# Kernel optimization log

Measured on AMD Instinct MI355X. Metric: run time of the kernel, lower is better.

## Reference

```python
import jax, jax.numpy as jnp
import numpy as np

N_NODES = 50000
N_EDGES = 800000
IN_CH = 128
OUT_CH = 128
LN_EPS = 1e-5


def setup_inputs() -> dict:
    key = jax.random.key(0)
    k1, k2, k3, k4 = jax.random.split(key, 4)
    x = jax.random.normal(k1, (N_NODES, IN_CH), dtype=jnp.float32)
    edge_index = jax.random.randint(k2, (2, N_EDGES), 0, N_NODES, dtype=jnp.int64)
    # GCNConv linear weight (glorot-ish scale) and bias
    W = jax.random.normal(k3, (IN_CH, OUT_CH), dtype=jnp.float32) * (1.0 / np.sqrt(IN_CH))
    b = jnp.zeros((OUT_CH,), dtype=jnp.float32)
    # LayerNorm affine params
    ln_w = jnp.ones((OUT_CH,), dtype=jnp.float32)
    ln_b = jnp.zeros((OUT_CH,), dtype=jnp.float32)
    del k4
    return {"x": x, "edge_index": edge_index, "W": W, "b": b, "ln_w": ln_w, "ln_b": ln_b}


def reference(x, edge_index, W, b, ln_w, ln_b):
    N = x.shape[0]
    # --- GCNConv: add self loops, symmetric normalization, scatter-add ---
    loop = jnp.arange(N, dtype=edge_index.dtype)
    row = jnp.concatenate([edge_index[0], loop])  # source nodes (x_j)
    col = jnp.concatenate([edge_index[1], loop])  # target nodes (aggregate here)
    h = x @ W  # [N, out]
    deg = jax.ops.segment_sum(jnp.ones(row.shape[0], dtype=h.dtype), col, num_segments=N)
    dinv = jnp.where(deg > 0, jax.lax.rsqrt(deg), 0.0)
    norm = dinv[row] * dinv[col]  # [E+N]
    msg = h[row] * norm[:, None]  # gather + scale
    out = jax.ops.segment_sum(msg, col, num_segments=N) + b  # scatter-add + bias
    # --- LayerNorm over feature dim ---
    mu = jnp.mean(out, axis=-1, keepdims=True)
    var = jnp.mean(jnp.square(out - mu), axis=-1, keepdims=True)
    out = (out - mu) * jax.lax.rsqrt(var + LN_EPS) * ln_w + ln_b
    # --- ReLU; dropout is identity in eval mode ---
    return jax.nn.relu(out)
```

## Files before the change

kernel.cpp:

```cpp
#include <hip/hip_runtime.h>
#include <hip/hip_bf16.h>

#define CH 128
#define LN_EPS 1e-5f
#define PBITS 8
#define CAP 8192

typedef unsigned int uint;
typedef unsigned short ushort;
typedef __attribute__((ext_vector_type(8))) short short8;
typedef __attribute__((ext_vector_type(4))) float f32x4;

__device__ __forceinline__ float bflo(uint v) { return __uint_as_float(v << 16); }
__device__ __forceinline__ float bfhi(uint v) { return __uint_as_float(v & 0xffff0000u); }
__device__ __forceinline__ ushort f2bf(float f) {
    uint u = __float_as_uint(f);
    u += 0x7fffu + ((u >> 16) & 1u);
    return (ushort)(u >> 16);
}

__global__ void k_init(const float* __restrict__ W, ushort* __restrict__ Wt,
                       uint* __restrict__ bcur) {
    if (blockIdx.x == 0) bcur[threadIdx.x] = 0;
    int o = blockIdx.x * 256 + threadIdx.x;
    int c = o >> 7, k = o & 127;
    Wt[o] = f2bf(W[k * CH + c]);
}

__global__ __launch_bounds__(256) void k_fused(const int* __restrict__ row,
                                               const int* __restrict__ col,
                                               uint* __restrict__ bk,
                                               uint* __restrict__ bcur,
                                               int E, int NB, int NBK,
                                               const float* __restrict__ x,
                                               const ushort* __restrict__ Wt,
                                               ushort* __restrict__ h, int N) {
    __shared__ __align__(16) char smem[49152];
    const int t = threadIdx.x;

    if ((int)blockIdx.x < NBK) {
        uint* cnt    = (uint*)smem;
        uint* startl = cnt + 256;
        uint* basel  = startl + 256;
        uint* wtot   = basel + 256;
        uint* sortv  = wtot + 4;
        int*  dstg   = (int*)(sortv + 4096);
        const int lane = t & 63, w = t >> 6;
        const int cs = blockIdx.x * 4096;
        const int m = min(4096, E - cs);

        cnt[t] = 0;
        __syncthreads();

        int  eb[16]; int erl[16]; uint ev[16];
#pragma unroll
        for (int k = 0; k < 16; ++k) {
            int i = t + k * 256;
            eb[k] = -1;
            if (i < m) {
                int c = col[cs + i];
                int r = row[cs + i];
                eb[k]  = c >> PBITS;
                ev[k]  = ((uint)(c & 255) << 16) | (uint)r;
                erl[k] = (int)atomicAdd(&cnt[eb[k]], 1u);
            }
        }
        __syncthreads();

        uint c0 = cnt[t];
        if (t < NB && c0) basel[t] = atomicAdd(&bcur[t], c0);
        uint s = c0;
#pragma unroll
        for (int d = 1; d < 64; d <<= 1) { uint v = __shfl_up(s, d); if (lane >= d) s += v; }
        if (lane == 63) wtot[w] = s;
        __syncthreads();
        uint pre = 0;
        for (int j = 0; j < w; ++j) pre += wtot[j];
        startl[t] = pre + s - c0;
        __syncthreads();

#pragma unroll
        for (int k = 0; k < 16; ++k) {
            if (eb[k] >= 0) {
                int pos = (int)startl[eb[k]] + erl[k];
                sortv[pos] = ev[k];
                dstg[pos]  = eb[k] * CAP + (int)basel[eb[k]] + erl[k];
            }
        }
        __syncthreads();

#pragma unroll
        for (int k = 0; k < 16; ++k) {
            int i = t + k * 256;
            if (i < m) bk[dstg[i]] = sortv[i];
        }
    } else {
        ushort* xs = (ushort*)smem;
        ushort* ws = xs + 64 * 128;
        const int bm = ((int)blockIdx.x - NBK) * 64;

#pragma unroll
        for (int i = 0; i < 8; ++i) {
            int gi = t + i * 256;
            int c = gi >> 4, g = gi & 15;
            uint4 v = *reinterpret_cast<const uint4*>(&Wt[gi * 8]);
            *reinterpret_cast<uint4*>(&ws[c * 128 + ((g ^ (c & 7)) << 3)]) = v;
        }
#pragma unroll
        for (int i = 0; i < 4; ++i) {
            int gi = t + i * 256;
            int r = gi >> 4, g = gi & 15;
            int rw = bm + r;
            uint4 p = make_uint4(0u, 0u, 0u, 0u);
            if (rw < N) {
                float4 va = *reinterpret_cast<const float4*>(&x[(size_t)rw * CH + g * 8]);
                float4 vb = *reinterpret_cast<const float4*>(&x[(size_t)rw * CH + g * 8 + 4]);
                p.x = ((uint)f2bf(va.y) << 16) | f2bf(va.x);
                p.y = ((uint)f2bf(va.w) << 16) | f2bf(va.z);
                p.z = ((uint)f2bf(vb.y) << 16) | f2bf(vb.x);
                p.w = ((uint)f2bf(vb.w) << 16) | f2bf(vb.z);
            }
            *reinterpret_cast<uint4*>(&xs[r * 128 + ((g ^ (r & 7)) << 3)]) = p;
        }
        __syncthreads();

        const int w  = t >> 6, l = t & 63;
        const int lr = l & 15;
        const int kg = l >> 4;
        f32x4 acc[8] = {};

#pragma unroll
        for (int s = 0; s < 4; ++s) {
            int g  = s * 4 + kg;
            int ar = w * 16 + lr;
            short8 a = *reinterpret_cast<const short8*>(&xs[ar * 128 + ((g ^ (ar & 7)) << 3)]);
#pragma unroll
            for (int c = 0; c < 8; ++c) {
                int bc = c * 16 + lr;
                short8 b = *reinterpret_cast<const short8*>(&ws[bc * 128 + ((g ^ (bc & 7)) << 3)]);
                acc[c] = __builtin_amdgcn_mfma_f32_16x16x32_bf16(a, b, acc[c], 0, 0, 0);
            }
        }

#pragma unroll
        for (int c = 0; c < 8; ++c)
#pragma unroll
            for (int j = 0; j < 4; ++j) {
                int rw = bm + w * 16 + kg * 4 + j;
                if (rw < N) h[(size_t)rw * CH + c * 16 + lr] = f2bf(acc[c][j]);
            }
    }
}

__global__ __launch_bounds__(256) void k_csr(const uint* __restrict__ bk,
                                             const uint* __restrict__ bcur,
                                             int* __restrict__ csr,
                                             int* __restrict__ deg,
                                             int* __restrict__ offs,
                                             float* __restrict__ dinv, int N) {
    __shared__ uint hist[256], startl[256], wtot[4];
    __shared__ ushort rls[CAP];
    const int t = threadIdx.x, lane = t & 63, w = t >> 6;
    const int b = blockIdx.x;
    const int base = b * CAP;
    const int cntb = (int)bcur[b];

    hist[t] = 0;
    __syncthreads();

    for (int i = t; i < cntb; i += 256) {
        uint v = bk[base + i];
        rls[i] = (ushort)atomicAdd(&hist[v >> 16], 1u);
    }
    __syncthreads();

    uint c0 = hist[t];
    uint s = c0;
#pragma unroll
    for (int d = 1; d < 64; d <<= 1) { uint v = __shfl_up(s, d); if (lane >= d) s += v; }
    if (lane == 63) wtot[w] = s;
    __syncthreads();
    uint pre = 0;
    for (int j = 0; j < w; ++j) pre += wtot[j];
    startl[t] = pre + s - c0;

    int node = (b << PBITS) + t;
    if (node < N) {
        deg[node]  = (int)c0;
        offs[node] = base + (int)(pre + s - c0);
        dinv[node] = rsqrtf((float)c0 + 1.0f);
    }
    __syncthreads();

    for (int i = t; i < cntb; i += 256) {
        uint v = bk[base + i];
        csr[base + (int)startl[v >> 16] + (int)rls[i]] = (int)(v & 0xffffu);
    }
}

__global__ __launch_bounds__(256) void k_agg(const uint2* __restrict__ hu2,
                                             const int* __restrict__ offs,
                                             const int* __restrict__ deg,
                                             const float* __restrict__ dinv,
                                             const int* __restrict__ csr,
                                             const float* __restrict__ bias,
                                             const float* __restrict__ lnw,
                                             const float* __restrict__ lnb,
                                             float* __restrict__ out, int N) {
    const int wave = threadIdx.x >> 6;
    const int lane = threadIdx.x & 63;
    const int half = lane >> 5;
    const int li   = lane & 31;
    const int n = blockIdx.x * 4 + wave;
    if (n >= N) return;

    const float di = dinv[n];
    const int start = offs[n];
    const int cnt = deg[n];

    float ax = 0.f, ay = 0.f, az = 0.f, aw = 0.f;
    if (half == 0) {
        uint2 sv = hu2[((size_t)n << 5) + li];
        float w = di * di;
        ax = bflo(sv.x) * w; ay = bfhi(sv.x) * w;
        az = bflo(sv.y) * w; aw = bfhi(sv.y) * w;
    }

    for (int base = 0; base < cnt; base += 64) {
        int m = cnt - base; if (m > 64) m = 64;
        int idx = 0; float dv = 0.f;
        if (lane < m) {
            idx = csr[start + base + lane];
            dv  = dinv[idx] * di;
        }
        for (int j = 0; j < m; j += 8) {
            int j0 = j + half;
            int   s0 = __shfl(idx, j0),     s1 = __shfl(idx, j0 + 2);
            int   s2 = __shfl(idx, j0 + 4), s3 = __shfl(idx, j0 + 6);
            float w0 = __shfl(dv, j0),      w1 = __shfl(dv, j0 + 2);
            float w2 = __shfl(dv, j0 + 4),  w3 = __shfl(dv, j0 + 6);
            uint2 v0 = hu2[((size_t)s0 << 5) + li];
            uint2 v1 = hu2[((size_t)s1 << 5) + li];
            uint2 v2 = hu2[((size_t)s2 << 5) + li];
            uint2 v3 = hu2[((size_t)s3 << 5) + li];
            ax = fmaf(bflo(v0.x), w0, ax); ay = fmaf(bfhi(v0.x), w0, ay);
            az = fmaf(bflo(v0.y), w0, az); aw = fmaf(bfhi(v0.y), w0, aw);
            ax = fmaf(bflo(v1.x), w1, ax); ay = fmaf(bfhi(v1.x), w1, ay);
            az = fmaf(bflo(v1.y), w1, az); aw = fmaf(bfhi(v1.y), w1, aw);
            ax = fmaf(bflo(v2.x), w2, ax); ay = fmaf(bfhi(v2.x), w2, ay);
            az = fmaf(bflo(v2.y), w2, az); aw = fmaf(bfhi(v2.y), w2, aw);
            ax = fmaf(bflo(v3.x), w3, ax); ay = fmaf(bfhi(v3.x), w3, ay);
            az = fmaf(bflo(v3.y), w3, az); aw = fmaf(bfhi(v3.y), w3, aw);
        }
    }

    ax += __shfl_xor(ax, 32); ay += __shfl_xor(ay, 32);
    az += __shfl_xor(az, 32); aw += __shfl_xor(aw, 32);

    float4 bb = reinterpret_cast<const float4*>(bias)[li];
    ax += bb.x; ay += bb.y; az += bb.z; aw += bb.w;

    float sum = ax + ay + az + aw;
    float sq  = ax * ax + ay * ay + az * az + aw * aw;
#pragma unroll
    for (int d = 16; d >= 1; d >>= 1) {
        sum += __shfl_xor(sum, d);
        sq  += __shfl_xor(sq, d);
    }
    float mean = sum * (1.0f / 128.0f);
    float var  = sq * (1.0f / 128.0f) - mean * mean;
    float rstd = rsqrtf(var + LN_EPS);

    if (half == 0) {
        float4 w4 = reinterpret_cast<const float4*>(lnw)[li];
        float4 b4 = reinterpret_cast<const float4*>(lnb)[li];
        float4 y;
        y.x = fmaxf((ax - mean) * rstd * w4.x + b4.x, 0.f);
        y.y = fmaxf((ay - mean) * rstd * w4.y + b4.y, 0.f);
        y.z = fmaxf((az - mean) * rstd * w4.z + b4.z, 0.f);
        y.w = fmaxf((aw - mean) * rstd * w4.w + b4.w, 0.f);
        reinterpret_cast<float4*>(out)[((size_t)n << 5) + li] = y;
    }
}

extern "C" void kernel_launch(void* const* d_in, const int* in_sizes, int n_in,
                              void* d_out, int out_size, void* d_ws, size_t ws_size,
                              hipStream_t stream) {
    const float* x   = (const float*)d_in[0];
    const int*   ei  = (const int*)d_in[1];
    const float* W   = (const float*)d_in[2];
    const float* b   = (const float*)d_in[3];
    const float* lnw = (const float*)d_in[4];
    const float* lnb = (const float*)d_in[5];
    float* out = (float*)d_out;

    const int N = in_sizes[0] / CH;
    const int E = in_sizes[1] / 2;
    const int NB  = (N + 255) >> PBITS;
    const int NBK = (E + 4095) / 4096;
    const int NG  = (N + 63) / 64;
    const int* row = ei;
    const int* col = ei + E;

    char* w8 = (char*)d_ws;
    ushort* h    = (ushort*)w8;
    int*   deg   = (int*)(w8 + (size_t)N * CH * 2);
    int*   offs  = deg + N;
    float* dinv  = (float*)(offs + N);
    uint*  bcur  = (uint*)(dinv + N);
    uint*  bk    = bcur + 256;
    int*   csr   = (int*)(bk + (size_t)NB * CAP);
    ushort* Wt   = (ushort*)(csr + (size_t)NB * CAP);

    k_init<<<CH * CH / 256, 256, 0, stream>>>(W, Wt, bcur);

    k_fused<<<NBK + NG, 256, 0, stream>>>(row, col, bk, bcur, E, NB, NBK,
                                          x, Wt, h, N);

    k_csr<<<NB, 256, 0, stream>>>(bk, bcur, csr, deg, offs, dinv, N);

    k_agg<<<(N + 3) / 4, 256, 0, stream>>>((const uint2*)h, offs, deg, dinv, csr,
                                           b, lnw, lnb, out, N);
}
```

Before: 71.37 us.

## Regroup stages: fuse CSR build with GEMM, drop W-transpose init kernel

Moves the bucket-scatter out of the fused kernel into its own launch and instead co-schedules the per-bucket CSR construction with the x@W GEMM blocks in one launch. The weight transpose/bf16 conversion kernel is removed; each GEMM block now reads fp32 W directly with strided column loads and converts into swizzled LDS. Counter zeroing becomes a memset. This keeps four launches but aims to overlap the CSR pass with the GEMM, at the cost of redundant, less-coalesced W reads in every GEMM block.

New measurement: 72.22 us. About the same (+1.2%).

```diff
diff --git a/kernel.cpp b/kernel.cpp
--- a/kernel.cpp
+++ b/kernel.cpp
@@ -19,56 +19,98 @@
     return (ushort)(u >> 16);
 }
 
-__global__ void k_init(const float* __restrict__ W, ushort* __restrict__ Wt,
-                       uint* __restrict__ bcur) {
-    if (blockIdx.x == 0) bcur[threadIdx.x] = 0;
-    int o = blockIdx.x * 256 + threadIdx.x;
-    int c = o >> 7, k = o & 127;
-    Wt[o] = f2bf(W[k * CH + c]);
-}
-
-__global__ __launch_bounds__(256) void k_fused(const int* __restrict__ row,
-                                               const int* __restrict__ col,
-                                               uint* __restrict__ bk,
-                                               uint* __restrict__ bcur,
-                                               int E, int NB, int NBK,
+__global__ __launch_bounds__(256) void k_bucket(const int* __restrict__ row,
+                                                const int* __restrict__ col,
+                                                uint* __restrict__ bk,
+                                                uint* __restrict__ bcur,
+                                                int E, int NB) {
+    __shared__ uint cnt[256], startl[256], basel[256], wtot[4];
+    __shared__ uint sortv[4096];
+    __shared__ int  dstg[4096];
+    const int t = threadIdx.x, lane = t & 63, w = t >> 6;
+    const int cs = blockIdx.x * 4096;
+    const int m = min(4096, E - cs);
+
+    cnt[t] = 0;
+    __syncthreads();
+
+    int  eb[16]; int erl[16]; uint ev[16];
+#pragma unroll
+    for (int k = 0; k < 16; ++k) {
+        int i = t + k * 256;
+        eb[k] = -1;
+        if (i < m) {
+            int c = col[cs + i];
+            int r = row[cs + i];
+            eb[k]  = c >> PBITS;
+            ev[k]  = ((uint)(c & 255) << 16) | (uint)r;
+            erl[k] = (int)atomicAdd(&cnt[eb[k]], 1u);
+        }
+    }
+    __syncthreads();
+
+    uint c0 = cnt[t];
+    if (t < NB && c0) basel[t] = atomicAdd(&bcur[t], c0);
+    uint s = c0;
+#pragma unroll
+    for (int d = 1; d < 64; d <<= 1) { uint v = __shfl_up(s, d); if (lane >= d) s += v; }
+    if (lane == 63) wtot[w] = s;
+    __syncthreads();
+    uint pre = 0;
+    for (int j = 0; j < w; ++j) pre += wtot[j];
+    startl[t] = pre + s - c0;
+    __syncthreads();
+
+#pragma unroll
+    for (int k = 0; k < 16; ++k) {
+        if (eb[k] >= 0) {
+            int pos = (int)startl[eb[k]] + erl[k];
+            sortv[pos] = ev[k];
+            dstg[pos]  = eb[k] * CAP + (int)basel[eb[k]] + erl[k];
+        }
+    }
+    __syncthreads();
+
+#pragma unroll
+    for (int k = 0; k < 16; ++k) {
+        int i = t + k * 256;
+        if (i < m) bk[dstg[i]] = sortv[i];
+    }
+}
+
+__global__ __launch_bounds__(256) void k_fused(const uint* __restrict__ bk,
+                                               const uint* __restrict__ bcur,
+                                               int* __restrict__ csr,
+                                               int* __restrict__ deg,
+                                               int* __restrict__ offs,
+                                               float* __restrict__ dinv,
+                                               int NB,
                                                const float* __restrict__ x,
-                                               const ushort* __restrict__ Wt,
+                                               const float* __restrict__ W,
                                                ushort* __restrict__ h, int N) {
     __shared__ __align__(16) char smem[49152];
     const int t = threadIdx.x;
 
-    if ((int)blockIdx.x < NBK) {
-        uint* cnt    = (uint*)smem;
-        uint* startl = cnt + 256;
-        uint* basel  = startl + 256;
-        uint* wtot   = basel + 256;
-        uint* sortv  = wtot + 4;
-        int*  dstg   = (int*)(sortv + 4096);
+    if ((int)blockIdx.x < NB) {
+        uint* hist   = (uint*)smem;
+        uint* startl = hist + 256;
+        uint* wtot   = startl + 256;
+        ushort* rls  = (ushort*)(wtot + 4);
         const int lane = t & 63, w = t >> 6;
-        const int cs = blockIdx.x * 4096;
-        const int m = min(4096, E - cs);
-
-        cnt[t] = 0;
-        __syncthreads();
-
-        int  eb[16]; int erl[16]; uint ev[16];
-#pragma unroll
-        for (int k = 0; k < 16; ++k) {
-            int i = t + k * 256;
-            eb[k] = -1;
-            if (i < m) {
-                int c = col[cs + i];
-                int r = row[cs + i];
-                eb[k]  = c >> PBITS;
-                ev[k]  = ((uint)(c & 255) << 16) | (uint)r;
-                erl[k] = (int)atomicAdd(&cnt[eb[k]], 1u);
-            }
-        }
-        __syncthreads();
-
-        uint c0 = cnt[t];
-        if (t < NB && c0) basel[t] = atomicAdd(&bcur[t], c0);
+        const int b = blockIdx.x;
+        const int base = b * CAP;
+        const int cntb = (int)bcur[b];
+
+        hist[t] = 0;
+        __syncthreads();
+
+        for (int i = t; i < cntb; i += 256) {
+            uint v = bk[base + i];
+            rls[i] = (ushort)atomicAdd(&hist[v >> 16], 1u);
+        }
+        __syncthreads();
+
+        uint c0 = hist[t];
         uint s = c0;
 #pragma unroll
         for (int d = 1; d < 64; d <<= 1) { uint v = __shfl_up(s, d); if (lane >= d) s += v; }
@@ -77,34 +119,40 @@
         uint pre = 0;
         for (int j = 0; j < w; ++j) pre += wtot[j];
         startl[t] = pre + s - c0;
-        __syncthreads();
-
-#pragma unroll
-        for (int k = 0; k < 16; ++k) {
-            if (eb[k] >= 0) {
-                int pos = (int)startl[eb[k]] + erl[k];
-                sortv[pos] = ev[k];
-                dstg[pos]  = eb[k] * CAP + (int)basel[eb[k]] + erl[k];
-            }
-        }
-        __syncthreads();
-
-#pragma unroll
-        for (int k = 0; k < 16; ++k) {
-            int i = t + k * 256;
-            if (i < m) bk[dstg[i]] = sortv[i];
+
+        int node = (b << PBITS) + t;
+        if (node < N) {
+            deg[node]  = (int)c0;
+            offs[node] = base + (int)(pre + s - c0);
+            dinv[node] = rsqrtf((float)c0 + 1.0f);
+        }
+        __syncthreads();
+
+        for (int i = t; i < cntb; i += 256) {
+            uint v = bk[base + i];
+            csr[base + (int)startl[v >> 16] + (int)rls[i]] = (int)(v & 0xffffu);
         }
     } else {
         ushort* xs = (ushort*)smem;
         ushort* ws = xs + 64 * 128;
-        const int bm = ((int)blockIdx.x - NBK) * 64;
-
-#pragma unroll
-        for (int i = 0; i < 8; ++i) {
-            int gi = t + i * 256;
-            int c = gi >> 4, g = gi & 15;
-            uint4 v = *reinterpret_cast<const uint4*>(&Wt[gi * 8]);
-            *reinterpret_cast<uint4*>(&ws[c * 128 + ((g ^ (c & 7)) << 3)]) = v;
+        const int bm = ((int)blockIdx.x - NB) * 64;
+
+        {
+            int c = t & 127, halfb = t >> 7;
+#pragma unroll
+            for (int i = 0; i < 8; ++i) {
+                int gg = halfb * 8 + i;
+                int kb = gg * 8;
+                uint u[4];
+#pragma unroll
+                for (int p = 0; p < 4; ++p) {
+                    float w0 = W[(size_t)(kb + 2 * p) * CH + c];
+                    float w1 = W[(size_t)(kb + 2 * p + 1) * CH + c];
+                    u[p] = ((uint)f2bf(w1) << 16) | f2bf(w0);
+                }
+                *reinterpret_cast<uint4*>(&ws[c * 128 + ((gg ^ (c & 7)) << 3)]) =
+                    *reinterpret_cast<uint4*>(u);
+            }
         }
 #pragma unroll
         for (int i = 0; i < 4; ++i) {
@@ -149,52 +197,6 @@
                 int rw = bm + w * 16 + kg * 4 + j;
                 if (rw < N) h[(size_t)rw * CH + c * 16 + lr] = f2bf(acc[c][j]);
             }
-    }
-}
-
-__global__ __launch_bounds__(256) void k_csr(const uint* __restrict__ bk,
-                                             const uint* __restrict__ bcur,
-                                             int* __restrict__ csr,
-                                             int* __restrict__ deg,
-                                             int* __restrict__ offs,
-                                             float* __restrict__ dinv, int N) {
-    __shared__ uint hist[256], startl[256], wtot[4];
-    __shared__ ushort rls[CAP];
-    const int t = threadIdx.x, lane = t & 63, w = t >> 6;
-    const int b = blockIdx.x;
-    const int base = b * CAP;
-    const int cntb = (int)bcur[b];
-
-    hist[t] = 0;
-    __syncthreads();
-
-    for (int i = t; i < cntb; i += 256) {
-        uint v = bk[base + i];
-        rls[i] = (ushort)atomicAdd(&hist[v >> 16], 1u);
-    }
-    __syncthreads();
-
-    uint c0 = hist[t];
-    uint s = c0;
-#pragma unroll
-    for (int d = 1; d < 64; d <<= 1) { uint v = __shfl_up(s, d); if (lane >= d) s += v; }
-    if (lane == 63) wtot[w] = s;
-    __syncthreads();
-    uint pre = 0;
-    for (int j = 0; j < w; ++j) pre += wtot[j];
-    startl[t] = pre + s - c0;
-
-    int node = (b << PBITS) + t;
-    if (node < N) {
-        deg[node]  = (int)c0;
-        offs[node] = base + (int)(pre + s - c0);
-        dinv[node] = rsqrtf((float)c0 + 1.0f);
-    }
-    __syncthreads();
-
-    for (int i = t; i < cntb; i += 256) {
-        uint v = bk[base + i];
-        csr[base + (int)startl[v >> 16] + (int)rls[i]] = (int)(v & 0xffffu);
     }
 }
 
@@ -310,14 +312,13 @@
     uint*  bcur  = (uint*)(dinv + N);
     uint*  bk    = bcur + 256;
     int*   csr   = (int*)(bk + (size_t)NB * CAP);
-    ushort* Wt   = (ushort*)(csr + (size_t)NB * CAP);
-
-    k_init<<<CH * CH / 256, 256, 0, stream>>>(W, Wt, bcur);
-
-    k_fused<<<NBK + NG, 256, 0, stream>>>(row, col, bk, bcur, E, NB, NBK,
-                                          x, Wt, h, N);
-
-    k_csr<<<NB, 256, 0, stream>>>(bk, bcur, csr, deg, offs, dinv, N);
+
+    hipMemsetAsync(bcur, 0, 256 * sizeof(uint), stream);
+
+    k_bucket<<<NBK, 256, 0, stream>>>(row, col, bk, bcur, E, NB);
+
+    k_fused<<<NB + NG, 256, 0, stream>>>(bk, bcur, csr, deg, offs, dinv, NB,
+                                         x, W, h, N);
 
     k_agg<<<(N + 3) / 4, 256, 0, stream>>>((const uint2*)h, offs, deg, dinv, csr,
                                            b, lnw, lnb, out, N);
```
